# Performance work log

Hardware: AMD Instinct MI355X
Metric: run time of the kernel (lower is better)

Reference implementation:

```python
import jax, jax.numpy as jnp
import numpy as np

RC = 5.0
N_ATYPE = 10
ACSF_NMU = 20
APSF_NMU = 10
ACSF_ETA = 100.0
APSF_ETA = 25.0
N_ATOMS = 30000
N_PAIRS = 200000
MAX_NB = 6
DENSE = 64
FEAT_DIM = ACSF_NMU * N_ATYPE + APSF_NMU * N_ATYPE + 22  # 322
ZINDEX = jnp.array([1.0, 3.0, 5.0, 6.0, 7.0, 8.0, 9.0, 11.0, 15.0, 16.0])
CHARGE_KEYS = jnp.array([0.0, 1.0, 3.0, 5.0, 6.0, 7.0, 8.0, 9.0, 11.0, 15.0, 16.0])
CHARGE_VALS = jnp.array([100000, 0, 1, 2, 3, 4, 5, 6, 7, 8, 9])


def pbc_shift(dr, box, box_inv):
    ds = dr @ box_inv
    ds = ds - jnp.floor(ds + 0.5)
    return ds @ box


def int_to_onehot(labels, num_classes):
    zidx = CHARGE_VALS[jnp.searchsorted(CHARGE_KEYS, labels)]
    return jax.nn.one_hot(zidx, num_classes, dtype=labels.dtype)


def dense_ln_relu(x, W, b, g, beta):
    h = x @ W + b
    mu = jnp.mean(h, axis=-1, keepdims=True)
    var = jnp.mean(jnp.square(h - mu), axis=-1, keepdims=True)
    return jax.nn.relu((h - mu) * jax.lax.rsqrt(var + 1e-6) * g + beta)


def forward(pos, box, valid_mask, W1, b1, g1, be1, W2, b2, g2, be2, W3, b3, g3, be3, Wo, bo,
            pairs, topo_nblist, topo_mask, mol_ID, atype_indices):
    dt = pos.dtype
    acsf_mus = jnp.linspace(0.0, 5.0, ACSF_NMU).astype(dt)
    apsf_mus = jnp.linspace(-1.0, 1.0, APSF_NMU).astype(dt)
    mScales = jnp.array([0.0, 0.0, 0.0, 0.0, 0.0, 1.0], dtype=dt)
    # regularize_pairs: padded pairs have i >= j, shift them off-diagonal
    p = pairs[:, :2]
    dp_flag = (p[:, 1] - p[:, 0] <= 0).astype(p.dtype)
    p = p - jnp.stack([dp_flag, 2 * dp_flag], axis=1)
    nbonds = pairs[:, 2]
    buffer_scales = (p[:, 0] < p[:, 1]).astype(dt) * valid_mask
    mscales = mScales[nbonds - 1] * buffer_scales  # computed as in original (unused downstream)
    box_inv = jnp.linalg.inv(box)
    ri = pos[p[:, 0]]
    rj = pos[p[:, 1]]
    rij = pbc_shift(rj - ri, box, box_inv)
    dr_norm = jnp.linalg.norm(rij + 1e-10, axis=1)
    same_mol = mol_ID[p[:, 0]] == mol_ID[p[:, 1]]
    buffer_inter = jnp.where(same_mol, 0.0, 1.0).astype(dt)
    cutoff = jnp.where(dr_norm <= RC, 0.5 * (1 + jnp.cos(jnp.pi * dr_norm / RC)), 0.0)
    buffer_nblist_inter_rc = buffer_inter * buffer_scales * cutoff
    # environment atoms of each pair endpoint (bonded topology neighbors)
    j_nb = topo_nblist[p[:, 0]]  # [P, M]
    k_nb = topo_nblist[p[:, 1]]
    j_mask = topo_mask[p[:, 0]] & (j_nb != -1) & (j_nb != p[:, 0:1]) & (j_nb != p[:, 1:2])
    k_mask = topo_mask[p[:, 1]] & (k_nb != -1) & (k_nb != p[:, 0:1]) & (k_nb != p[:, 1:2])
    rij_unit = rij / (dr_norm[:, None] + 1e-10)

    def cos_gamma(center, nb, mask, unit):
        r_env = jnp.where(mask[..., None], pos[nb], 0.0)  # [P, M, 3]
        rX = pbc_shift(r_env - center[:, None, :], box, box_inv)
        rXn = rX / jnp.linalg.norm(rX + 1e-10, axis=2, keepdims=True)
        return jnp.einsum('pmi,pi->pm', rXn, unit) * mask

    cos_gamma_i = cos_gamma(ri, j_nb, j_mask, rij_unit)
    cos_gamma_j = cos_gamma(rj, k_nb, k_mask, -rij_unit)
    type_cols = jnp.arange(N_ATYPE)

    def apsf(cg, nb, mask):
        feat = jnp.exp(-APSF_ETA * jnp.square(cg[..., None] - apsf_mus)) * mask[..., None]
        onehot = (atype_indices[nb][..., None] == type_cols).astype(dt)
        return jnp.einsum('pmk,pml->pkl', feat, onehot)  # [P, APSF_NMU, N_ATYPE]

    G_pair = (apsf(cos_gamma_i, j_nb, j_mask) + apsf(cos_gamma_j, k_nb, k_mask)) * 0.5 \
             * buffer_nblist_inter_rc[:, None, None]
    # ACSF radial atom-centered features
    r_env = pos[topo_nblist]  # [N, M, 3]
    dr = pbc_shift(r_env - pos[:, None, :], box, box_inv)
    dnorm = jnp.linalg.norm(dr + 1e-10, axis=2)
    fx = dnorm / RC
    f_cut = jnp.where(fx < 1, 0.5 * (jnp.cos(jnp.pi * fx) + 1), 0.0) * topo_mask
    G_raw = jnp.exp(-ACSF_ETA * jnp.square(dnorm[..., None] - acsf_mus)) * f_cut[..., None]
    nb_onehot = (atype_indices[topo_nblist][..., None] == type_cols).astype(dt)
    G_atom = jnp.einsum('nmk,nml->nkl', G_raw, nb_onehot)  # [N, ACSF_NMU, N_ATYPE]
    atom_feat = 0.5 * (G_atom[p[:, 0]] + G_atom[p[:, 1]])
    # element charge + one-hot block
    elem = ZINDEX[atype_indices].astype(dt)
    j_z = elem[p[:, 0]]
    k_z = elem[p[:, 1]]
    atype_onehot = jnp.concatenate([j_z[:, None], int_to_onehot(j_z, 10),
                                    k_z[:, None], int_to_onehot(k_z, 10)], axis=1)
    feats = jnp.concatenate([atom_feat.reshape(atom_feat.shape[0], -1),
                             G_pair.reshape(G_pair.shape[0], -1),
                             atype_onehot], axis=1)  # [P, 322]
    # MLP energy head
    x = dense_ln_relu(feats, W1, b1, g1, be1)
    x = dense_ln_relu(x, W2, b2, g2, be2)
    x = dense_ln_relu(x, W3, b3, g3, be3)
    out_AB = x @ Wo + bo
    return jnp.sum(out_AB * buffer_nblist_inter_rc[:, None])


def setup_inputs() -> dict:
    key = jax.random.key(0)
    ks = jax.random.split(key, 16)
    L = 30.0
    pos = jax.random.uniform(ks[0], (N_ATOMS, 3), jnp.float32, 0.0, L)
    box = jnp.eye(3, dtype=jnp.float32) * L
    i = jax.random.randint(ks[1], (N_PAIRS,), 2, N_ATOMS)
    j = jax.random.randint(ks[2], (N_PAIRS,), 2, N_ATOMS)
    p0 = jnp.minimum(i, j)
    p1 = jnp.maximum(i, j)
    pairs = jnp.stack([p0, p1, jnp.full((N_PAIRS,), 6, dtype=p0.dtype)], axis=1)
    valid_mask = (jax.random.uniform(ks[3], (N_PAIRS,)) < 0.95).astype(jnp.float32)
    nb = jax.random.randint(ks[4], (N_ATOMS, MAX_NB), 0, N_ATOMS)
    topo_nblist = jnp.where(jax.random.uniform(ks[5], (N_ATOMS, MAX_NB)) < 0.25, -1, nb)
    topo_mask = topo_nblist != -1
    mol_ID = jnp.arange(N_ATOMS, dtype=jnp.int32) // 3
    atype_indices = jax.random.randint(ks[6], (N_ATOMS,), 0, N_ATYPE)

    def dense_w(k, fin, fout):
        return jax.random.normal(k, (fin, fout), jnp.float32) / np.float32(np.sqrt(fin))

    return {
        'pos': pos, 'box': box, 'valid_mask': valid_mask,
        'W1': dense_w(ks[7], FEAT_DIM, DENSE), 'b1': jnp.zeros((DENSE,), jnp.float32),
        'g1': jnp.ones((DENSE,), jnp.float32), 'be1': jnp.zeros((DENSE,), jnp.float32),
        'W2': dense_w(ks[8], DENSE, DENSE), 'b2': jnp.zeros((DENSE,), jnp.float32),
        'g2': jnp.ones((DENSE,), jnp.float32), 'be2': jnp.zeros((DENSE,), jnp.float32),
        'W3': dense_w(ks[9], DENSE, DENSE), 'b3': jnp.zeros((DENSE,), jnp.float32),
        'g3': jnp.ones((DENSE,), jnp.float32), 'be3': jnp.zeros((DENSE,), jnp.float32),
        'Wo': dense_w(ks[10], DENSE, 1), 'bo': jnp.zeros((1,), jnp.float32),
        'pairs': pairs, 'topo_nblist': topo_nblist, 'topo_mask': topo_mask,
        'mol_ID': mol_ID, 'atype_indices': atype_indices,
    }


def reference(pos, box, valid_mask, W1, b1, g1, be1, W2, b2, g2, be2, W3, b3, g3, be3, Wo, bo,
              pairs, topo_nblist, topo_mask, mol_ID, atype_indices):
    return forward(pos, box, valid_mask, W1, b1, g1, be1, W2, b2, g2, be2, W3, b3, g3, be3, Wo, bo,
                   pairs, topo_nblist, topo_mask, mol_ID, atype_indices)
```

## Files before the change

kernel.cpp:

```cpp
#include <hip/hip_runtime.h>
#include <math.h>

#define N_PAIRS_C 200000
#define MAX_NB_C 6
#define RC_F 5.0f
#define PI_F 3.14159265358979323846f
#define NBLK 256
#define NTHR 1024
#define SLICE 782
#define LCAP 160
#define W1S 332
#define W23S 68
#define FPAD 324

__device__ __constant__ float c_ZIND[10] = {1.f, 3.f, 5.f, 6.f, 7.f, 8.f, 9.f, 11.f, 15.f, 16.f};

__device__ __forceinline__ void invert3x3(const float* b, float* inv) {
    float a00 = b[0], a01 = b[1], a02 = b[2];
    float a10 = b[3], a11 = b[4], a12 = b[5];
    float a20 = b[6], a21 = b[7], a22 = b[8];
    float det = a00 * (a11 * a22 - a12 * a21)
              - a01 * (a10 * a22 - a12 * a20)
              + a02 * (a10 * a21 - a11 * a20);
    float id = 1.0f / det;
    inv[0] =  (a11 * a22 - a12 * a21) * id;
    inv[1] = -(a01 * a22 - a02 * a21) * id;
    inv[2] =  (a01 * a12 - a02 * a11) * id;
    inv[3] = -(a10 * a22 - a12 * a20) * id;
    inv[4] =  (a00 * a22 - a02 * a20) * id;
    inv[5] = -(a00 * a12 - a02 * a10) * id;
    inv[6] =  (a10 * a21 - a11 * a20) * id;
    inv[7] = -(a00 * a21 - a01 * a20) * id;
    inv[8] =  (a00 * a11 - a01 * a10) * id;
}

__device__ __forceinline__ void pbc3(float dx, float dy, float dz,
                                     const float* box, const float* binv,
                                     float& ox, float& oy, float& oz) {
    float s0 = dx * binv[0] + dy * binv[3] + dz * binv[6];
    float s1 = dx * binv[1] + dy * binv[4] + dz * binv[7];
    float s2 = dx * binv[2] + dy * binv[5] + dz * binv[8];
    s0 -= floorf(s0 + 0.5f);
    s1 -= floorf(s1 + 0.5f);
    s2 -= floorf(s2 + 0.5f);
    ox = s0 * box[0] + s1 * box[3] + s2 * box[6];
    oy = s0 * box[1] + s1 * box[4] + s2 * box[7];
    oz = s0 * box[2] + s1 * box[5] + s2 * box[8];
}

__device__ __forceinline__ float wsum64(float v) {
    #pragma unroll
    for (int off = 32; off > 0; off >>= 1) v += __shfl_xor(v, off, 64);
    return v;
}

__device__ __forceinline__ float ln_relu(float h, float g, float be) {
    float mu = wsum64(h) * 0.015625f;
    float d  = h - mu;
    float var = wsum64(d * d) * 0.015625f;
    float r = d * (1.0f / sqrtf(var + 1e-6f)) * g + be;
    return fmaxf(r, 0.0f);
}

__global__ __launch_bounds__(NTHR, 4) void fused_kernel(
    const float* __restrict__ pos,
    const float* __restrict__ box,
    const float* __restrict__ valid_mask,
    const float* __restrict__ W1, const float* __restrict__ b1,
    const float* __restrict__ g1, const float* __restrict__ be1,
    const float* __restrict__ W2, const float* __restrict__ b2,
    const float* __restrict__ g2, const float* __restrict__ be2,
    const float* __restrict__ W3, const float* __restrict__ b3,
    const float* __restrict__ g3, const float* __restrict__ be3,
    const float* __restrict__ Wo, const float* __restrict__ bo,
    const int* __restrict__ pairs,
    const int* __restrict__ nblist,
    const int* __restrict__ atype,
    const int* __restrict__ mol_ID,
    float* __restrict__ out) {

    __shared__ __align__(16) float W1t[64][W1S];
    __shared__ __align__(16) float W2t[64][W23S];
    __shared__ __align__(16) float W3t[64][W23S];
    __shared__ __align__(16) float feats[16][FPAD];
    __shared__ __align__(16) float xb[16][64];
    __shared__ int   l_p0[LCAP], l_p1[LCAP];
    __shared__ float l_fac[LCAP];
    __shared__ int   l_cnt;
    __shared__ float wacc[16];

    const int tid = threadIdx.x;
    const int w = tid >> 6;
    const int j = tid & 63;

    if (tid == 0) l_cnt = 0;

    float bx[9], bi[9];
    #pragma unroll
    for (int i = 0; i < 9; ++i) bx[i] = box[i];
    invert3x3(bx, bi);

    __syncthreads();

    {
        const int roto = blockIdx.x % 81;
        #pragma unroll
        for (int r = 0; r < 6; ++r) {
            int gi = w + 16 * r;
            if (gi < 81) {
                gi += roto; if (gi >= 81) gi -= 81;
                int f0 = 4 * gi;
                float4 v;
                v.x = (f0 + 0 < 322) ? W1[(f0 + 0) * 64 + j] : 0.0f;
                v.y = (f0 + 1 < 322) ? W1[(f0 + 1) * 64 + j] : 0.0f;
                v.z = (f0 + 2 < 322) ? W1[(f0 + 2) * 64 + j] : 0.0f;
                v.w = (f0 + 3 < 322) ? W1[(f0 + 3) * 64 + j] : 0.0f;
                *(float4*)&W1t[j][f0] = v;
            }
        }
        {
            int f0 = 4 * w;
            float4 v2, v3;
            v2.x = W2[(f0 + 0) * 64 + j]; v3.x = W3[(f0 + 0) * 64 + j];
            v2.y = W2[(f0 + 1) * 64 + j]; v3.y = W3[(f0 + 1) * 64 + j];
            v2.z = W2[(f0 + 2) * 64 + j]; v3.z = W3[(f0 + 2) * 64 + j];
            v2.w = W2[(f0 + 3) * 64 + j]; v3.w = W3[(f0 + 3) * 64 + j];
            *(float4*)&W2t[j][f0] = v2;
            *(float4*)&W3t[j][f0] = v3;
        }
    }

    if (tid < SLICE) {
        int t = blockIdx.x * SLICE + tid;
        if (t < N_PAIRS_C) {
            int i0 = pairs[3 * t], i1 = pairs[3 * t + 1];
            int dp = (i1 - i0 <= 0) ? 1 : 0;
            int p0 = i0 - dp, p1 = i1 - 2 * dp;
            if (p0 < p1) {
                float vm = valid_mask[t];
                if (vm != 0.0f && mol_ID[p0] != mol_ID[p1]) {
                    float dx, dy, dz;
                    pbc3(pos[3 * p1] - pos[3 * p0],
                         pos[3 * p1 + 1] - pos[3 * p0 + 1],
                         pos[3 * p1 + 2] - pos[3 * p0 + 2], bx, bi, dx, dy, dz);
                    float ax = dx + 1e-10f, ay = dy + 1e-10f, az = dz + 1e-10f;
                    float dn = sqrtf(ax * ax + ay * ay + az * az);
                    if (dn <= RC_F) {
                        float fac = vm * 0.5f * (1.0f + __cosf(PI_F * dn / RC_F));
                        int slot = atomicAdd(&l_cnt, 1);
                        if (slot < LCAP) {
                            l_p0[slot] = p0; l_p1[slot] = p1; l_fac[slot] = fac;
                        }
                    }
                }
            }
        }
    }
    __syncthreads();

    int cnt = l_cnt;
    if (cnt > LCAP) cnt = LCAP;
    const int rounds = (cnt + 15) >> 4;

    const float b1j = b1[j], g1j = g1[j], be1j = be1[j];
    const float b2j = b2[j], g2j = g2[j], be2j = be2[j];
    const float b3j = b3[j], g3j = g3[j], be3j = be3[j];
    const float woj = Wo[j], bo0 = bo[0];

    float acc = 0.0f;

    if (w < 8 && rounds > 0) {
        float* frowA = &feats[2 * w][0];
        float* frowB = &feats[2 * w + 1][0];
        float* xbA = &xb[2 * w][0];
        float* xbB = &xb[2 * w + 1][0];

        auto featurize = [&](int idx, float* frow) -> float {
            bool val = idx < cnt;
            int ci = val ? idx : 0;
            int p0 = l_p0[ci];
            int p1 = l_p1[ci];
            float fac = val ? l_fac[ci] : 0.0f;

            float rix = pos[3 * p0], riy = pos[3 * p0 + 1], riz = pos[3 * p0 + 2];
            float rjx = pos[3 * p1], rjy = pos[3 * p1 + 1], rjz = pos[3 * p1 + 2];
            float dxr, dyr, dzr;
            pbc3(rjx - rix, rjy - riy, rjz - riz, bx, bi, dxr, dyr, dzr);
            float axr = dxr + 1e-10f, ayr = dyr + 1e-10f, azr = dzr + 1e-10f;
            float dn0 = sqrtf(axr * axr + ayr * ayr + azr * azr);
            float idn = 1.0f / (dn0 + 1e-10f);
            float ux = dxr * idn, uy = dyr * idn, uz = dzr * idn;

            float sdn = 1.0f, sfc = 0.0f, scg = 0.0f;
            int smeta = 0;
            if (j < 12) {
                int side = (j >= 6) ? 1 : 0;
                int m = side ? (j - 6) : j;
                int a = side ? p1 : p0;
                int nb = nblist[a * MAX_NB_C + m];
                if (nb != -1) {
                    float cx = side ? rjx : rix;
                    float cy = side ? rjy : riy;
                    float cz = side ? rjz : riz;
                    float ex, ey, ez;
                    pbc3(pos[3 * nb] - cx, pos[3 * nb + 1] - cy, pos[3 * nb + 2] - cz,
                         bx, bi, ex, ey, ez);
                    float nx = ex + 1e-10f, ny = ey + 1e-10f, nz = ez + 1e-10f;
                    sdn = sqrtf(nx * nx + ny * ny + nz * nz);
                    float fr = sdn * (1.0f / RC_F);
                    sfc = (fr < 1.0f) ? 0.5f * (__cosf(PI_F * fr) + 1.0f) : 0.0f;
                    int pv = (nb != p0 && nb != p1) ? 1 : 0;
                    smeta = atype[nb] | (1 << 8) | (pv << 9);
                    float sgn = side ? -1.0f : 1.0f;
                    scg = sgn * (ex * ux + ey * uy + ez * uz) / sdn;
                }
            }

            float4 z = make_float4(0.f, 0.f, 0.f, 0.f);
            *(float4*)&frow[4 * j] = z;
            if (j < 17) *(float4*)&frow[256 + 4 * j] = z;
            if (j == 12) { int ti = atype[p0]; frow[300] = c_ZIND[ti]; frow[301 + ti] = 1.0f; }
            if (j == 13) { int tj2 = atype[p1]; frow[311] = c_ZIND[tj2]; frow[312 + tj2] = 1.0f; }

            #pragma unroll
            for (int it = 0; it < 6; ++it) {
                int task = j + 64 * it;
                if (task < 360) {
                    int s, k;
                    bool acs = (task < 240);
                    if (acs) { s = task / 20; k = task - s * 20; }
                    else     { int t2 = task - 240; s = t2 / 10; k = t2 - s * 10; }
                    float dn_s = __shfl(sdn, s);
                    float fc_s = __shfl(sfc, s);
                    float cg_s = __shfl(scg, s);
                    int meta_s = __shfl(smeta, s);
                    int ty_s = meta_s & 0xff;
                    if (acs) {
                        if ((meta_s & 0x100) && fc_s != 0.0f) {
                            float mu = (5.0f * (float)k) / 19.0f;
                            float d = dn_s - mu;
                            atomicAdd(&frow[k * 10 + ty_s], 0.5f * __expf(-100.0f * d * d) * fc_s);
                        }
                    } else {
                        if (meta_s & 0x200) {
                            float mu = -1.0f + (2.0f * (float)k) / 9.0f;
                            float d = cg_s - mu;
                            atomicAdd(&frow[200 + k * 10 + ty_s], 0.5f * fac * __expf(-25.0f * d * d));
                        }
                    }
                }
            }
            return fac;
        };

        for (int r = 0; r < rounds; ++r) {
            float facA = featurize((r << 4) + 2 * w + 0, frowA);
            float facB = featurize((r << 4) + 2 * w + 1, frowB);
            asm volatile("s_waitcnt lgkmcnt(0)" ::: "memory");

            const float4* wr1 = (const float4*)&W1t[j][0];
            const float4* fA4 = (const float4*)frowA;
            const float4* fB4 = (const float4*)frowB;
            float hA = b1j, hB = b1j;
            #pragma unroll 3
            for (int g = 0; g < 81; ++g) {
                float4 wv = wr1[g];
                float4 a = fA4[g], b = fB4[g];
                hA = fmaf(a.x, wv.x, hA); hA = fmaf(a.y, wv.y, hA);
                hA = fmaf(a.z, wv.z, hA); hA = fmaf(a.w, wv.w, hA);
                hB = fmaf(b.x, wv.x, hB); hB = fmaf(b.y, wv.y, hB);
                hB = fmaf(b.z, wv.z, hB); hB = fmaf(b.w, wv.w, hB);
            }
            float x1A = ln_relu(hA, g1j, be1j);
            float x1B = ln_relu(hB, g1j, be1j);
            xbA[j] = x1A; xbB[j] = x1B;

            const float4* xA4 = (const float4*)xbA;
            const float4* xB4 = (const float4*)xbB;
            float h2A = b2j, h2B = b2j;
            #pragma unroll
            for (int g = 0; g < 16; ++g) {
                float4 wv = *(const float4*)&W2t[j][4 * g];
                float4 a = xA4[g], b = xB4[g];
                h2A = fmaf(a.x, wv.x, h2A); h2A = fmaf(a.y, wv.y, h2A);
                h2A = fmaf(a.z, wv.z, h2A); h2A = fmaf(a.w, wv.w, h2A);
                h2B = fmaf(b.x, wv.x, h2B); h2B = fmaf(b.y, wv.y, h2B);
                h2B = fmaf(b.z, wv.z, h2B); h2B = fmaf(b.w, wv.w, h2B);
            }
            float x2A = ln_relu(h2A, g2j, be2j);
            float x2B = ln_relu(h2B, g2j, be2j);
            xbA[j] = x2A; xbB[j] = x2B;

            float h3A = b3j, h3B = b3j;
            #pragma unroll
            for (int g = 0; g < 16; ++g) {
                float4 wv = *(const float4*)&W3t[j][4 * g];
                float4 a = xA4[g], b = xB4[g];
                h3A = fmaf(a.x, wv.x, h3A); h3A = fmaf(a.y, wv.y, h3A);
                h3A = fmaf(a.z, wv.z, h3A); h3A = fmaf(a.w, wv.w, h3A);
                h3B = fmaf(b.x, wv.x, h3B); h3B = fmaf(b.y, wv.y, h3B);
                h3B = fmaf(b.z, wv.z, h3B); h3B = fmaf(b.w, wv.w, h3B);
            }
            float x3A = ln_relu(h3A, g3j, be3j);
            float x3B = ln_relu(h3B, g3j, be3j);

            float rA = wsum64(x3A * woj);
            float rB = wsum64(x3B * woj);
            if (j == 0) acc += (rA + bo0) * facA + (rB + bo0) * facB;
        }
    }

    if (j == 0) wacc[w] = acc;
    __syncthreads();
    if (w == 0) {
        float v = (j < 16) ? wacc[j] : 0.0f;
        v = wsum64(v);
        if (j == 0) atomicAdd(out, v);
    }
}

extern "C" void kernel_launch(void* const* d_in, const int* in_sizes, int n_in,
                              void* d_out, int out_size, void* d_ws, size_t ws_size,
                              hipStream_t stream) {
    const float* pos        = (const float*)d_in[0];
    const float* box        = (const float*)d_in[1];
    const float* valid_mask = (const float*)d_in[2];
    const float* W1  = (const float*)d_in[3];
    const float* b1  = (const float*)d_in[4];
    const float* g1  = (const float*)d_in[5];
    const float* be1 = (const float*)d_in[6];
    const float* W2  = (const float*)d_in[7];
    const float* b2  = (const float*)d_in[8];
    const float* g2  = (const float*)d_in[9];
    const float* be2 = (const float*)d_in[10];
    const float* W3  = (const float*)d_in[11];
    const float* b3  = (const float*)d_in[12];
    const float* g3  = (const float*)d_in[13];
    const float* be3 = (const float*)d_in[14];
    const float* Wo  = (const float*)d_in[15];
    const float* bo  = (const float*)d_in[16];
    const int* pairs = (const int*)d_in[17];
    const int* nbl   = (const int*)d_in[18];
    const int* mol   = (const int*)d_in[20];
    const int* aty   = (const int*)d_in[21];

    float* out = (float*)d_out;

    hipMemsetAsync(out, 0, sizeof(float), stream);
    fused_kernel<<<NBLK, NTHR, 0, stream>>>(
        pos, box, valid_mask,
        W1, b1, g1, be1, W2, b2, g2, be2, W3, b3, g3, be3, Wo, bo,
        pairs, nbl, aty, mol, out);
}
```

Baseline: 41.16 us.

## Split pair filtering into separate kernel and compute features in registers via readlane

Moves pair filtering into a standalone kernel that compacts surviving pairs into a global workspace list through a global atomic counter. The MLP kernel then grid-strides over that list, so per-block load balancing no longer depends on a fixed pair slice with a capped local buffer. Features are built per lane in registers, each lane owning five feature slots, and read with readlane instead of going through shared-memory atomics and buffers. The cost is an extra kernel launch and a global round trip for the compacted records.

Measured after the change: 150.6 us. 266% more time.

```diff
diff --git a/kernel.cpp b/kernel.cpp
--- a/kernel.cpp
+++ b/kernel.cpp
@@ -5,13 +5,12 @@
 #define MAX_NB_C 6
 #define RC_F 5.0f
 #define PI_F 3.14159265358979323846f
+#define FILT_THREADS 256
+#define FILT_BLOCKS ((N_PAIRS_C + FILT_THREADS - 1) / FILT_THREADS)
 #define NBLK 256
 #define NTHR 1024
-#define SLICE 782
-#define LCAP 160
-#define W1S 332
+#define W1S 324
 #define W23S 68
-#define FPAD 324
 
 __device__ __constant__ float c_ZIND[10] = {1.f, 3.f, 5.f, 6.f, 7.f, 8.f, 9.f, 11.f, 15.f, 16.f};
 
@@ -62,10 +61,69 @@
     return fmaxf(r, 0.0f);
 }
 
-__global__ __launch_bounds__(NTHR, 4) void fused_kernel(
+__device__ __forceinline__ float rlf(float v, int lane) {
+    return __int_as_float(__builtin_amdgcn_readlane(__float_as_int(v), lane));
+}
+__device__ __forceinline__ int rli(int v, int lane) {
+    return __builtin_amdgcn_readlane(v, lane);
+}
+
+__global__ __launch_bounds__(FILT_THREADS) void filter_kernel(
+        const float* __restrict__ pos,
+        const float* __restrict__ box,
+        const float* __restrict__ valid_mask,
+        const int* __restrict__ pairs,
+        const int* __restrict__ mol_ID,
+        int* __restrict__ counter,
+        int4* __restrict__ recs,
+        int max_active,
+        float* __restrict__ out) {
+    __shared__ int l_cnt, l_base;
+    __shared__ int4 srec[FILT_THREADS];
+    const int tid = threadIdx.x;
+    if (tid == 0) l_cnt = 0;
+    if (blockIdx.x == 0 && tid == 0) out[0] = 0.0f;
+    __syncthreads();
+
+    float bx[9], bi[9];
+    #pragma unroll
+    for (int i = 0; i < 9; ++i) bx[i] = box[i];
+    invert3x3(bx, bi);
+
+    int t = blockIdx.x * FILT_THREADS + tid;
+    if (t < N_PAIRS_C) {
+        int i0 = pairs[3 * t], i1 = pairs[3 * t + 1];
+        int dp = (i1 - i0 <= 0) ? 1 : 0;
+        int p0 = i0 - dp, p1 = i1 - 2 * dp;
+        if (p0 < p1) {
+            float vm = valid_mask[t];
+            if (vm != 0.0f && mol_ID[p0] != mol_ID[p1]) {
+                float dx, dy, dz;
+                pbc3(pos[3 * p1] - pos[3 * p0],
+                     pos[3 * p1 + 1] - pos[3 * p0 + 1],
+                     pos[3 * p1 + 2] - pos[3 * p0 + 2], bx, bi, dx, dy, dz);
+                float ax = dx + 1e-10f, ay = dy + 1e-10f, az = dz + 1e-10f;
+                float dn = sqrtf(ax * ax + ay * ay + az * az);
+                if (dn <= RC_F) {
+                    float fac = vm * 0.5f * (1.0f + __cosf(PI_F * dn / RC_F));
+                    int slot = atomicAdd(&l_cnt, 1);
+                    srec[slot] = make_int4(p0, p1, __float_as_int(fac), 0);
+                }
+            }
+        }
+    }
+    __syncthreads();
+    if (tid == 0) l_base = (l_cnt > 0) ? atomicAdd(counter, l_cnt) : 0;
+    __syncthreads();
+    if (tid < l_cnt) {
+        int g = l_base + tid;
+        if (g < max_active) recs[g] = srec[tid];
+    }
+}
+
+__global__ __launch_bounds__(NTHR, 4) void mlp_kernel(
     const float* __restrict__ pos,
     const float* __restrict__ box,
-    const float* __restrict__ valid_mask,
     const float* __restrict__ W1, const float* __restrict__ b1,
     const float* __restrict__ g1, const float* __restrict__ be1,
     const float* __restrict__ W2, const float* __restrict__ b2,
@@ -73,43 +131,28 @@
     const float* __restrict__ W3, const float* __restrict__ b3,
     const float* __restrict__ g3, const float* __restrict__ be3,
     const float* __restrict__ Wo, const float* __restrict__ bo,
-    const int* __restrict__ pairs,
     const int* __restrict__ nblist,
     const int* __restrict__ atype,
-    const int* __restrict__ mol_ID,
+    const int* __restrict__ counter,
+    const int4* __restrict__ recs,
+    int max_active,
     float* __restrict__ out) {
 
     __shared__ __align__(16) float W1t[64][W1S];
     __shared__ __align__(16) float W2t[64][W23S];
     __shared__ __align__(16) float W3t[64][W23S];
-    __shared__ __align__(16) float feats[16][FPAD];
-    __shared__ __align__(16) float xb[16][64];
-    __shared__ int   l_p0[LCAP], l_p1[LCAP];
-    __shared__ float l_fac[LCAP];
-    __shared__ int   l_cnt;
     __shared__ float wacc[16];
 
     const int tid = threadIdx.x;
     const int w = tid >> 6;
     const int j = tid & 63;
 
-    if (tid == 0) l_cnt = 0;
-
-    float bx[9], bi[9];
-    #pragma unroll
-    for (int i = 0; i < 9; ++i) bx[i] = box[i];
-    invert3x3(bx, bi);
-
-    __syncthreads();
-
     {
-        const int roto = blockIdx.x % 81;
         #pragma unroll
-        for (int r = 0; r < 6; ++r) {
-            int gi = w + 16 * r;
-            if (gi < 81) {
-                gi += roto; if (gi >= 81) gi -= 81;
-                int f0 = 4 * gi;
+        for (int i = 0; i < 6; ++i) {
+            int q = w + 16 * i;
+            if (q < 81) {
+                int f0 = 4 * q;
                 float4 v;
                 v.x = (f0 + 0 < 322) ? W1[(f0 + 0) * 64 + j] : 0.0f;
                 v.y = (f0 + 1 < 322) ? W1[(f0 + 1) * 64 + j] : 0.0f;
@@ -130,176 +173,183 @@
         }
     }
 
-    if (tid < SLICE) {
-        int t = blockIdx.x * SLICE + tid;
-        if (t < N_PAIRS_C) {
-            int i0 = pairs[3 * t], i1 = pairs[3 * t + 1];
-            int dp = (i1 - i0 <= 0) ? 1 : 0;
-            int p0 = i0 - dp, p1 = i1 - 2 * dp;
-            if (p0 < p1) {
-                float vm = valid_mask[t];
-                if (vm != 0.0f && mol_ID[p0] != mol_ID[p1]) {
-                    float dx, dy, dz;
-                    pbc3(pos[3 * p1] - pos[3 * p0],
-                         pos[3 * p1 + 1] - pos[3 * p0 + 1],
-                         pos[3 * p1 + 2] - pos[3 * p0 + 2], bx, bi, dx, dy, dz);
-                    float ax = dx + 1e-10f, ay = dy + 1e-10f, az = dz + 1e-10f;
-                    float dn = sqrtf(ax * ax + ay * ay + az * az);
-                    if (dn <= RC_F) {
-                        float fac = vm * 0.5f * (1.0f + __cosf(PI_F * dn / RC_F));
-                        int slot = atomicAdd(&l_cnt, 1);
-                        if (slot < LCAP) {
-                            l_p0[slot] = p0; l_p1[slot] = p1; l_fac[slot] = fac;
-                        }
-                    }
-                }
-            }
-        }
-    }
-    __syncthreads();
-
-    int cnt = l_cnt;
-    if (cnt > LCAP) cnt = LCAP;
-    const int rounds = (cnt + 15) >> 4;
+    int count = *counter;
+    if (count > max_active) count = max_active;
+    const int nch = (count + 15) >> 4;
+
+    float bx[9], bi[9];
+    #pragma unroll
+    for (int i = 0; i < 9; ++i) bx[i] = box[i];
+    invert3x3(bx, bi);
+
+    float mu_[5], eta_[5];
+    int ty_[5], sel_[5];
+    #pragma unroll
+    for (int r = 0; r < 5; ++r) {
+        int F = j + 64 * r;
+        if (F < 200)      { mu_[r] = 5.0f * (float)(F / 10) / 19.0f; eta_[r] = -100.0f; ty_[r] = F % 10; sel_[r] = 1; }
+        else if (F < 300) { int G = F - 200; mu_[r] = -1.0f + 2.0f * (float)(G / 10) / 9.0f; eta_[r] = -25.0f; ty_[r] = G % 10; sel_[r] = 0; }
+        else              { mu_[r] = 0.0f; eta_[r] = 0.0f; ty_[r] = 255; sel_[r] = 0; }
+    }
 
     const float b1j = b1[j], g1j = g1[j], be1j = be1[j];
     const float b2j = b2[j], g2j = g2[j], be2j = be2[j];
     const float b3j = b3[j], g3j = g3[j], be3j = be3[j];
     const float woj = Wo[j], bo0 = bo[0];
 
+    __syncthreads();
+
     float acc = 0.0f;
 
-    if (w < 8 && rounds > 0) {
-        float* frowA = &feats[2 * w][0];
-        float* frowB = &feats[2 * w + 1][0];
-        float* xbA = &xb[2 * w][0];
-        float* xbB = &xb[2 * w + 1][0];
-
-        auto featurize = [&](int idx, float* frow) -> float {
-            bool val = idx < cnt;
-            int ci = val ? idx : 0;
-            int p0 = l_p0[ci];
-            int p1 = l_p1[ci];
-            float fac = val ? l_fac[ci] : 0.0f;
-
-            float rix = pos[3 * p0], riy = pos[3 * p0 + 1], riz = pos[3 * p0 + 2];
-            float rjx = pos[3 * p1], rjy = pos[3 * p1 + 1], rjz = pos[3 * p1 + 2];
-            float dxr, dyr, dzr;
-            pbc3(rjx - rix, rjy - riy, rjz - riz, bx, bi, dxr, dyr, dzr);
-            float axr = dxr + 1e-10f, ayr = dyr + 1e-10f, azr = dzr + 1e-10f;
-            float dn0 = sqrtf(axr * axr + ayr * ayr + azr * azr);
-            float idn = 1.0f / (dn0 + 1e-10f);
-            float ux = dxr * idn, uy = dyr * idn, uz = dzr * idn;
-
-            float sdn = 1.0f, sfc = 0.0f, scg = 0.0f;
-            int smeta = 0;
-            if (j < 12) {
-                int side = (j >= 6) ? 1 : 0;
-                int m = side ? (j - 6) : j;
-                int a = side ? p1 : p0;
-                int nb = nblist[a * MAX_NB_C + m];
-                if (nb != -1) {
-                    float cx = side ? rjx : rix;
-                    float cy = side ? rjy : riy;
-                    float cz = side ? rjz : riz;
-                    float ex, ey, ez;
-                    pbc3(pos[3 * nb] - cx, pos[3 * nb + 1] - cy, pos[3 * nb + 2] - cz,
-                         bx, bi, ex, ey, ez);
-                    float nx = ex + 1e-10f, ny = ey + 1e-10f, nz = ez + 1e-10f;
-                    sdn = sqrtf(nx * nx + ny * ny + nz * nz);
-                    float fr = sdn * (1.0f / RC_F);
-                    sfc = (fr < 1.0f) ? 0.5f * (__cosf(PI_F * fr) + 1.0f) : 0.0f;
-                    int pv = (nb != p0 && nb != p1) ? 1 : 0;
-                    smeta = atype[nb] | (1 << 8) | (pv << 9);
-                    float sgn = side ? -1.0f : 1.0f;
-                    scg = sgn * (ex * ux + ey * uy + ez * uz) / sdn;
-                }
-            }
-
-            float4 z = make_float4(0.f, 0.f, 0.f, 0.f);
-            *(float4*)&frow[4 * j] = z;
-            if (j < 17) *(float4*)&frow[256 + 4 * j] = z;
-            if (j == 12) { int ti = atype[p0]; frow[300] = c_ZIND[ti]; frow[301 + ti] = 1.0f; }
-            if (j == 13) { int tj2 = atype[p1]; frow[311] = c_ZIND[tj2]; frow[312 + tj2] = 1.0f; }
-
-            #pragma unroll
-            for (int it = 0; it < 6; ++it) {
-                int task = j + 64 * it;
-                if (task < 360) {
-                    int s, k;
-                    bool acs = (task < 240);
-                    if (acs) { s = task / 20; k = task - s * 20; }
-                    else     { int t2 = task - 240; s = t2 / 10; k = t2 - s * 10; }
-                    float dn_s = __shfl(sdn, s);
-                    float fc_s = __shfl(sfc, s);
-                    float cg_s = __shfl(scg, s);
-                    int meta_s = __shfl(smeta, s);
-                    int ty_s = meta_s & 0xff;
-                    if (acs) {
-                        if ((meta_s & 0x100) && fc_s != 0.0f) {
-                            float mu = (5.0f * (float)k) / 19.0f;
-                            float d = dn_s - mu;
-                            atomicAdd(&frow[k * 10 + ty_s], 0.5f * __expf(-100.0f * d * d) * fc_s);
-                        }
-                    } else {
-                        if (meta_s & 0x200) {
-                            float mu = -1.0f + (2.0f * (float)k) / 9.0f;
-                            float d = cg_s - mu;
-                            atomicAdd(&frow[200 + k * 10 + ty_s], 0.5f * fac * __expf(-25.0f * d * d));
-                        }
+    if (w < 8) {
+        for (int chunk = blockIdx.x; chunk < nch; chunk += NBLK) {
+            int iA = chunk * 16 + 2 * w;
+            int iB = iA + 1;
+            int4 recA = (iA < count) ? recs[iA] : make_int4(0, 0, 0, 0);
+            int4 recB = (iB < count) ? recs[iB] : make_int4(0, 0, 0, 0);
+            int p0A = recA.x, p1A = recA.y; float facA = __int_as_float(recA.z);
+            int p0B = recB.x, p1B = recB.y; float facB = __int_as_float(recB.z);
+
+            float sdn = 1.0f, sfce = 0.0f, scg = 0.0f, sapw = 0.0f;
+            int sty = 0;
+            {
+                bool isA = (j < 12);
+                bool isB = (j >= 16 && j < 28);
+                if (isA || isB) {
+                    int s  = isA ? j : (j - 16);
+                    int p0 = isA ? p0A : p0B;
+                    int p1 = isA ? p1A : p1B;
+                    float fac = isA ? facA : facB;
+                    float rix = pos[3 * p0], riy = pos[3 * p0 + 1], riz = pos[3 * p0 + 2];
+                    float rjx = pos[3 * p1], rjy = pos[3 * p1 + 1], rjz = pos[3 * p1 + 2];
+                    float dxr, dyr, dzr;
+                    pbc3(rjx - rix, rjy - riy, rjz - riz, bx, bi, dxr, dyr, dzr);
+                    float axr = dxr + 1e-10f, ayr = dyr + 1e-10f, azr = dzr + 1e-10f;
+                    float dn0 = sqrtf(axr * axr + ayr * ayr + azr * azr);
+                    float idn = 1.0f / (dn0 + 1e-10f);
+                    float ux = dxr * idn, uy = dyr * idn, uz = dzr * idn;
+                    int side = (s >= 6) ? 1 : 0;
+                    int m = side ? (s - 6) : s;
+                    int a = side ? p1 : p0;
+                    int nb = nblist[a * MAX_NB_C + m];
+                    if (nb != -1) {
+                        float cx = side ? rjx : rix;
+                        float cy = side ? rjy : riy;
+                        float cz = side ? rjz : riz;
+                        float ex, ey, ez;
+                        pbc3(pos[3 * nb] - cx, pos[3 * nb + 1] - cy, pos[3 * nb + 2] - cz,
+                             bx, bi, ex, ey, ez);
+                        float nx = ex + 1e-10f, ny = ey + 1e-10f, nz = ez + 1e-10f;
+                        float dn = sqrtf(nx * nx + ny * ny + nz * nz);
+                        float fr = dn * (1.0f / RC_F);
+                        float fc = (fr < 1.0f) ? 0.5f * (__cosf(PI_F * fr) + 1.0f) : 0.0f;
+                        sdn = dn;
+                        sfce = 0.5f * fc;
+                        sty = atype[nb];
+                        int pv = (nb != p0 && nb != p1) ? 1 : 0;
+                        float sgn = side ? -1.0f : 1.0f;
+                        scg = sgn * (ex * ux + ey * uy + ez * uz) / dn;
+                        sapw = pv ? 0.5f * fac : 0.0f;
                     }
                 }
             }
-            return fac;
-        };
-
-        for (int r = 0; r < rounds; ++r) {
-            float facA = featurize((r << 4) + 2 * w + 0, frowA);
-            float facB = featurize((r << 4) + 2 * w + 1, frowB);
-            asm volatile("s_waitcnt lgkmcnt(0)" ::: "memory");
-
-            const float4* wr1 = (const float4*)&W1t[j][0];
-            const float4* fA4 = (const float4*)frowA;
-            const float4* fB4 = (const float4*)frowB;
+
+            float frA[6] = {0.f, 0.f, 0.f, 0.f, 0.f, 0.f};
+            float frB[6] = {0.f, 0.f, 0.f, 0.f, 0.f, 0.f};
+            #pragma unroll
+            for (int s = 0; s < 12; ++s) {
+                float adn = rlf(sdn, s),      afce = rlf(sfce, s);
+                float acg = rlf(scg, s),      aapw = rlf(sapw, s);
+                int   aty = rli(sty, s);
+                float bdn = rlf(sdn, 16 + s), bfce = rlf(sfce, 16 + s);
+                float bcg = rlf(scg, 16 + s), bapw = rlf(sapw, 16 + s);
+                int   bty = rli(sty, 16 + s);
+                #pragma unroll
+                for (int r = 0; r < 5; ++r) {
+                    float xa = sel_[r] ? adn : acg;
+                    float wa = sel_[r] ? afce : aapw;
+                    float ta = xa - mu_[r];
+                    frA[r] += ((aty == ty_[r]) ? wa : 0.0f) * __expf(eta_[r] * ta * ta);
+                    float xb = sel_[r] ? bdn : bcg;
+                    float wb = sel_[r] ? bfce : bapw;
+                    float tb = xb - mu_[r];
+                    frB[r] += ((bty == ty_[r]) ? wb : 0.0f) * __expf(eta_[r] * tb * tb);
+                }
+            }
+            {
+                int tiA = atype[p0A], tjA = atype[p1A];
+                int tiB = atype[p0B], tjB = atype[p1B];
+                if (j >= 44) {
+                    int oh = j - 44;
+                    float vA, vB;
+                    if (oh == 0)       { vA = c_ZIND[tiA];              vB = c_ZIND[tiB]; }
+                    else if (oh <= 10) { vA = (tiA == oh - 1) ? 1.f : 0.f; vB = (tiB == oh - 1) ? 1.f : 0.f; }
+                    else if (oh == 11) { vA = c_ZIND[tjA];              vB = c_ZIND[tjB]; }
+                    else               { vA = (tjA == oh - 12) ? 1.f : 0.f; vB = (tjB == oh - 12) ? 1.f : 0.f; }
+                    frA[4] = vA; frB[4] = vB;
+                }
+                if (j == 0) { frA[5] = (tjA == 8) ? 1.f : 0.f; frB[5] = (tjB == 8) ? 1.f : 0.f; }
+                if (j == 1) { frA[5] = (tjA == 9) ? 1.f : 0.f; frB[5] = (tjB == 9) ? 1.f : 0.f; }
+            }
+
             float hA = b1j, hB = b1j;
-            #pragma unroll 3
-            for (int g = 0; g < 81; ++g) {
-                float4 wv = wr1[g];
-                float4 a = fA4[g], b = fB4[g];
-                hA = fmaf(a.x, wv.x, hA); hA = fmaf(a.y, wv.y, hA);
-                hA = fmaf(a.z, wv.z, hA); hA = fmaf(a.w, wv.w, hA);
-                hB = fmaf(b.x, wv.x, hB); hB = fmaf(b.y, wv.y, hB);
-                hB = fmaf(b.z, wv.z, hB); hB = fmaf(b.w, wv.w, hB);
+            #pragma unroll
+            for (int r = 0; r < 5; ++r) {
+                const float4* wrow = (const float4*)&W1t[j][64 * r];
+                #pragma unroll
+                for (int gg = 0; gg < 16; ++gg) {
+                    float4 wv = wrow[gg];
+                    int l0 = 4 * gg;
+                    hA = fmaf(rlf(frA[r], l0 + 0), wv.x, hA);
+                    hA = fmaf(rlf(frA[r], l0 + 1), wv.y, hA);
+                    hA = fmaf(rlf(frA[r], l0 + 2), wv.z, hA);
+                    hA = fmaf(rlf(frA[r], l0 + 3), wv.w, hA);
+                    hB = fmaf(rlf(frB[r], l0 + 0), wv.x, hB);
+                    hB = fmaf(rlf(frB[r], l0 + 1), wv.y, hB);
+                    hB = fmaf(rlf(frB[r], l0 + 2), wv.z, hB);
+                    hB = fmaf(rlf(frB[r], l0 + 3), wv.w, hB);
+                }
+            }
+            {
+                float2 wt = *(const float2*)&W1t[j][320];
+                hA = fmaf(rlf(frA[5], 0), wt.x, hA);
+                hA = fmaf(rlf(frA[5], 1), wt.y, hA);
+                hB = fmaf(rlf(frB[5], 0), wt.x, hB);
+                hB = fmaf(rlf(frB[5], 1), wt.y, hB);
             }
             float x1A = ln_relu(hA, g1j, be1j);
             float x1B = ln_relu(hB, g1j, be1j);
-            xbA[j] = x1A; xbB[j] = x1B;
-
-            const float4* xA4 = (const float4*)xbA;
-            const float4* xB4 = (const float4*)xbB;
+
             float h2A = b2j, h2B = b2j;
             #pragma unroll
-            for (int g = 0; g < 16; ++g) {
-                float4 wv = *(const float4*)&W2t[j][4 * g];
-                float4 a = xA4[g], b = xB4[g];
-                h2A = fmaf(a.x, wv.x, h2A); h2A = fmaf(a.y, wv.y, h2A);
-                h2A = fmaf(a.z, wv.z, h2A); h2A = fmaf(a.w, wv.w, h2A);
-                h2B = fmaf(b.x, wv.x, h2B); h2B = fmaf(b.y, wv.y, h2B);
-                h2B = fmaf(b.z, wv.z, h2B); h2B = fmaf(b.w, wv.w, h2B);
+            for (int gg = 0; gg < 16; ++gg) {
+                float4 wv = *(const float4*)&W2t[j][4 * gg];
+                int l0 = 4 * gg;
+                h2A = fmaf(rlf(x1A, l0 + 0), wv.x, h2A);
+                h2A = fmaf(rlf(x1A, l0 + 1), wv.y, h2A);
+                h2A = fmaf(rlf(x1A, l0 + 2), wv.z, h2A);
+                h2A = fmaf(rlf(x1A, l0 + 3), wv.w, h2A);
+                h2B = fmaf(rlf(x1B, l0 + 0), wv.x, h2B);
+                h2B = fmaf(rlf(x1B, l0 + 1), wv.y, h2B);
+                h2B = fmaf(rlf(x1B, l0 + 2), wv.z, h2B);
+                h2B = fmaf(rlf(x1B, l0 + 3), wv.w, h2B);
             }
             float x2A = ln_relu(h2A, g2j, be2j);
             float x2B = ln_relu(h2B, g2j, be2j);
-            xbA[j] = x2A; xbB[j] = x2B;
 
             float h3A = b3j, h3B = b3j;
             #pragma unroll
-            for (int g = 0; g < 16; ++g) {
-                float4 wv = *(const float4*)&W3t[j][4 * g];
-                float4 a = xA4[g], b = xB4[g];
-                h3A = fmaf(a.x, wv.x, h3A); h3A = fmaf(a.y, wv.y, h3A);
-                h3A = fmaf(a.z, wv.z, h3A); h3A = fmaf(a.w, wv.w, h3A);
-                h3B = fmaf(b.x, wv.x, h3B); h3B = fmaf(b.y, wv.y, h3B);
-                h3B = fmaf(b.z, wv.z, h3B); h3B = fmaf(b.w, wv.w, h3B);
+            for (int gg = 0; gg < 16; ++gg) {
+                float4 wv = *(const float4*)&W3t[j][4 * gg];
+                int l0 = 4 * gg;
+                h3A = fmaf(rlf(x2A, l0 + 0), wv.x, h3A);
+                h3A = fmaf(rlf(x2A, l0 + 1), wv.y, h3A);
+                h3A = fmaf(rlf(x2A, l0 + 2), wv.z, h3A);
+                h3A = fmaf(rlf(x2A, l0 + 3), wv.w, h3A);
+                h3B = fmaf(rlf(x2B, l0 + 0), wv.x, h3B);
+                h3B = fmaf(rlf(x2B, l0 + 1), wv.y, h3B);
+                h3B = fmaf(rlf(x2B, l0 + 2), wv.z, h3B);
+                h3B = fmaf(rlf(x2B, l0 + 3), wv.w, h3B);
             }
             float x3A = ln_relu(h3A, g3j, be3j);
             float x3B = ln_relu(h3B, g3j, be3j);
@@ -315,7 +365,8 @@
     if (w == 0) {
         float v = (j < 16) ? wacc[j] : 0.0f;
         v = wsum64(v);
-        if (j == 0) atomicAdd(out, v);
+        if (j == 0 && v != 0.0f) atomicAdd(out, v);
+        else if (j == 0 && blockIdx.x == 0) atomicAdd(out, v);
     }
 }
 
@@ -344,11 +395,20 @@
     const int* mol   = (const int*)d_in[20];
     const int* aty   = (const int*)d_in[21];
 
+    char* ws = (char*)d_ws;
+    int* counter = (int*)ws;
+    int4* recs   = (int4*)(ws + 256);
+    long long cap_ll = ((long long)ws_size - 256) / 16;
+    int cap = (cap_ll > 0) ? (int)cap_ll : 0;
+    if (cap > N_PAIRS_C) cap = N_PAIRS_C;
+
     float* out = (float*)d_out;
 
-    hipMemsetAsync(out, 0, sizeof(float), stream);
-    fused_kernel<<<NBLK, NTHR, 0, stream>>>(
-        pos, box, valid_mask,
+    hipMemsetAsync(counter, 0, sizeof(int), stream);
+    filter_kernel<<<FILT_BLOCKS, FILT_THREADS, 0, stream>>>(
+        pos, box, valid_mask, pairs, mol, counter, recs, cap, out);
+    mlp_kernel<<<NBLK, NTHR, 0, stream>>>(
+        pos, box,
         W1, b1, g1, be1, W2, b2, g2, be2, W3, b3, g3, be3, Wo, bo,
-        pairs, nbl, aty, mol, out);
-}
+        nbl, aty, counter, recs, cap, out);
+}
```
